# Optimization experiments

Measured on AMD Instinct MI355X. Metric: run time of the kernel, lower is better.

Reference implementation:

```python
import jax, jax.numpy as jnp
import numpy as np

B, L, D, H, E, K = 1, 512, 512, 512, 32, 2

def setup_inputs() -> dict:
    key = jax.random.key(0)
    ks = jax.random.split(key, 6)
    x = jax.random.normal(ks[0], (B, L, D), dtype=jnp.float32)
    router_scale = 1.0 + 0.02 * jax.random.normal(ks[1], (D,), dtype=jnp.float32)
    router_logits_w = 0.02 * jax.random.normal(ks[2], (D, E), dtype=jnp.float32)
    gating_einsum = 0.02 * jax.random.normal(ks[3], (E, 2, H, D), dtype=jnp.float32)
    linear_w = 0.02 * jax.random.normal(ks[4], (E, H, D), dtype=jnp.float32)
    per_expert_scale = 1.0 + 0.02 * jax.random.normal(ks[5], (E,), dtype=jnp.float32)
    return {"x": x, "router_scale": router_scale, "router_logits_w": router_logits_w,
            "gating_einsum": gating_einsum, "linear_w": linear_w,
            "per_expert_scale": per_expert_scale}

def reference(x, router_scale, router_logits_w, gating_einsum, linear_w, per_expert_scale):
    d = x.shape[-1]
    n_experts = router_logits_w.shape[-1]
    # RMSNorm without scale (fp32)
    x32 = x.astype(jnp.float32)
    var = jnp.mean(jnp.square(x32), axis=-1, keepdims=True)
    router_input = x32 * jax.lax.rsqrt(var + 1e-6)
    root_size = jax.lax.rsqrt(jnp.asarray(d, dtype=router_input.dtype))
    router_input = router_input * root_size * router_scale.astype(router_input.dtype)
    logits = jnp.dot(router_input, router_logits_w).astype(jnp.float32)  # [B,L,E]
    probs = jax.nn.softmax(logits, axis=-1)
    _, top_k_indices = jax.lax.top_k(logits, K)  # [B,L,K]
    indicator = jax.nn.one_hot(top_k_indices, n_experts, dtype=probs.dtype).sum(axis=-2)
    gate_weights = indicator * probs
    renorm = jnp.sum(gate_weights, axis=-1, keepdims=True)
    renorm = jnp.where(renorm > 0.0, renorm, 1.0)
    weights = probs / renorm
    top_k_weights = jnp.take_along_axis(weights, top_k_indices, axis=-1)  # [B,L,K]
    output = jnp.zeros_like(x)
    for ki in range(K):  # small fixed k; faithful to source's per-slot gather
        expert_idx = top_k_indices[:, :, ki]          # [B,L] int32
        expert_w = top_k_weights[:, :, ki]            # [B,L]
        gate_params = gating_einsum[expert_idx]       # [B,L,2,H,D] -- the big gather
        lin_params = linear_w[expert_idx]             # [B,L,H,D]
        escale = per_expert_scale[expert_idx]         # [B,L]
        gate_0 = jnp.einsum('bld,blhd->blh', x, gate_params[:, :, 0])
        gate_1 = jnp.einsum('bld,blhd->blh', x, gate_params[:, :, 1])
        activated = jax.nn.gelu(gate_0) * gate_1
        expert_out = jnp.einsum('blh,blhd->bld', activated, lin_params)
        output = output + expert_out * (escale * expert_w)[..., None]
    return output
```

## Files before the change

kernel.cpp:

```cpp
#include <hip/hip_runtime.h>
#include <hip/hip_bf16.h>
#include <math.h>

#define LTOK 512
#define DDIM 512
#define NEXP 32
#define HDIM 512

typedef __attribute__((ext_vector_type(8))) short short8;
typedef __attribute__((ext_vector_type(4))) float floatx4;

__device__ __forceinline__ unsigned bpack(float a, float b) {
    unsigned ua = __float_as_uint(a), ub = __float_as_uint(b);
    ua += 0x7FFFu + ((ua >> 16) & 1u);
    ub += 0x7FFFu + ((ub >> 16) & 1u);
    return (ua >> 16) | (ub & 0xFFFF0000u);
}


__global__ __launch_bounds__(64) void router_kernel(
    const float* __restrict__ x, const float* __restrict__ rs,
    const float* __restrict__ Wr, const float* __restrict__ pes,
    int* __restrict__ cnt, int* __restrict__ alist, float* __restrict__ slist,
    short* __restrict__ xb)
{
    const int t = blockIdx.x;
    const int lane = threadIdx.x;

    float xv[8];
    float ss = 0.f;
#pragma unroll
    for (int j = 0; j < 8; ++j) {
        xv[j] = x[t * DDIM + j * 64 + lane];
        ss += xv[j] * xv[j];
    }
#pragma unroll
    for (int j = 0; j < 8; ++j)
        xb[t * DDIM + j * 64 + lane] = (short)(bpack(xv[j], 0.f) & 0xFFFFu);

#pragma unroll
    for (int o = 32; o > 0; o >>= 1) ss += __shfl_xor(ss, o);
    const float var = ss * (1.0f / 512.0f);
    const float coef = rsqrtf(var + 1e-6f) * rsqrtf(512.0f);

    __shared__ float ri[DDIM];
#pragma unroll
    for (int j = 0; j < 8; ++j) {
        const int d = j * 64 + lane;
        ri[d] = xv[j] * coef * rs[d];
    }
    __syncthreads();

    const int e = lane & 31;
    const int half = lane >> 5;
    const int dbeg = half * 256;
    float l0 = 0.f, l1 = 0.f, l2 = 0.f, l3 = 0.f;
#pragma unroll 4
    for (int d = dbeg; d < dbeg + 256; d += 4) {
        l0 = fmaf(ri[d + 0], Wr[(d + 0) * NEXP + e], l0);
        l1 = fmaf(ri[d + 1], Wr[(d + 1) * NEXP + e], l1);
        l2 = fmaf(ri[d + 2], Wr[(d + 2) * NEXP + e], l2);
        l3 = fmaf(ri[d + 3], Wr[(d + 3) * NEXP + e], l3);
    }
    float lg = (l0 + l1) + (l2 + l3);
    lg += __shfl_xor(lg, 32);

    __shared__ float lgs[NEXP];
    if (lane < 32) lgs[lane] = lg;
    __syncthreads();

    if (lane == 0) {
        int i0 = 0; float m0 = lgs[0];
        for (int i = 1; i < NEXP; ++i) if (lgs[i] > m0) { m0 = lgs[i]; i0 = i; }
        int i1 = -1; float m1 = -1e30f;
        for (int i = 0; i < NEXP; ++i) if (i != i0 && lgs[i] > m1) { m1 = lgs[i]; i1 = i; }
        const float e1 = expf(m1 - m0);
        const float inv = 1.0f / (1.0f + e1);
        const float w0 = inv, w1 = e1 * inv;

        int p0 = atomicAdd(&cnt[i0], 1);
        alist[i0 * LTOK + p0] = t * 2;
        slist[i0 * LTOK + p0] = w0 * pes[i0];
        int p1 = atomicAdd(&cnt[i1], 1);
        alist[i1 * LTOK + p1] = t * 2 + 1;
        slist[i1 * LTOK + p1] = w1 * pes[i1];
    }
}

__global__ __launch_bounds__(256, 4) void gates_kernel(
    const short* __restrict__ xb, const float* __restrict__ G,
    const int* __restrict__ cnt, const int* __restrict__ alist,
    short* __restrict__ act)
{
    const int e  = blockIdx.y;
    const int h0 = blockIdx.x * 16;
    const int Ne = cnt[e];
    if (Ne == 0) return;
    const int wv   = threadIdx.x >> 6;
    const int g    = wv & 1;
    const int kh   = wv >> 1;
    const int lane = threadIdx.x & 63;
    const int n    = lane & 15;
    const int quad = lane >> 4;

    __shared__ float red[4][2][4][64];

    const float* Grow = G + ((size_t)((e * 2 + g) * HDIM) + h0 + n) * DDIM + kh * 256;
    const short* xbh  = xb + kh * 256;
    const int* al = alist + e * LTOK;

    short8 Bf[8];
#pragma unroll
    for (int ks = 0; ks < 8; ++ks) {
        const int ko = ks * 32 + quad * 8;
        const floatx4 b0 = *(const floatx4*)(Grow + ko);
        const floatx4 b1 = *(const floatx4*)(Grow + ko + 4);
        union { short8 s; unsigned u[4]; } B;
        B.u[0] = bpack(b0.x, b0.y);
        B.u[1] = bpack(b0.z, b0.w);
        B.u[2] = bpack(b1.x, b1.y);
        B.u[3] = bpack(b1.z, b1.w);
        Bf[ks] = B.s;
    }

    for (int mb = 0; mb < Ne; mb += 32) {
        int arow[2];
#pragma unroll
        for (int i = 0; i < 2; ++i) {
            int s = mb + i * 16 + n;
            arow[i] = al[s < Ne ? s : Ne - 1] >> 1;
        }
        floatx4 acc[2] = {};

#pragma unroll
        for (int ks = 0; ks < 8; ++ks) {
            const int ko = ks * 32 + quad * 8;
#pragma unroll
            for (int i = 0; i < 2; ++i) {
                const short8 A = *(const short8*)(xbh + (size_t)arow[i] * DDIM + ko);
                acc[i] = __builtin_amdgcn_mfma_f32_16x16x32_bf16(A, Bf[ks], acc[i], 0, 0, 0);
            }
        }

#pragma unroll
        for (int i = 0; i < 2; ++i)
#pragma unroll
            for (int r = 0; r < 4; ++r)
                red[wv][i][r][lane] = acc[i][r];
        __syncthreads();

        {
            const int i = wv & 1;
            const int u = wv >> 1;
#pragma unroll
            for (int rr = 0; rr < 2; ++rr) {
                const int r = u * 2 + rr;
                const int s = mb + i * 16 + quad * 4 + r;
                if (s < Ne) {
                    const int a = al[s];
                    const float g0 = red[0][i][r][lane] + red[2][i][r][lane];
                    const float g1 = red[1][i][r][lane] + red[3][i][r][lane];
                    const float uu = 0.7978845608f * (g0 + 0.044715f * g0 * g0 * g0);
                    const float sg = 1.0f / (1.0f + __expf(-2.0f * uu));
                    const float v = g0 * sg * g1;
                    act[(size_t)a * HDIM + h0 + n] = (short)(bpack(v, 0.f) & 0xFFFFu);
                }
            }
        }
        __syncthreads();
    }
}

__global__ __launch_bounds__(256, 4) void linear_kernel(
    const short* __restrict__ act, const float* __restrict__ Wl,
    const int* __restrict__ cnt, const int* __restrict__ alist,
    const float* __restrict__ slist, float* __restrict__ yb)
{
    const int e  = blockIdx.y;
    const int d0 = blockIdx.x * 16;
    const int Ne = cnt[e];
    if (Ne == 0) return;
    const int wv   = threadIdx.x >> 6;
    const int lane = threadIdx.x & 63;
    const int n    = lane & 15;
    const int quad = lane >> 4;

    __shared__ float red[4][2][4][64];

    const float* Wcol = Wl + (size_t)e * HDIM * DDIM + d0 + n;
    const int* al = alist + e * LTOK;
    const float* sl = slist + e * LTOK;

    short8 Bf[4];
#pragma unroll
    for (int ks = 0; ks < 4; ++ks) {
        const int ko = wv * 128 + ks * 32 + quad * 8;
        float w[8];
#pragma unroll
        for (int j = 0; j < 8; ++j)
            w[j] = Wcol[(size_t)(ko + j) * DDIM];
        union { short8 s; unsigned u[4]; } B;
        B.u[0] = bpack(w[0], w[1]);
        B.u[1] = bpack(w[2], w[3]);
        B.u[2] = bpack(w[4], w[5]);
        B.u[3] = bpack(w[6], w[7]);
        Bf[ks] = B.s;
    }

    for (int mb = 0; mb < Ne; mb += 32) {
        int arow[2];
#pragma unroll
        for (int i = 0; i < 2; ++i) {
            int s = mb + i * 16 + n;
            arow[i] = al[s < Ne ? s : Ne - 1];
        }
        floatx4 acc[2] = {};

#pragma unroll
        for (int ks = 0; ks < 4; ++ks) {
            const int ko = wv * 128 + ks * 32 + quad * 8;
#pragma unroll
            for (int i = 0; i < 2; ++i) {
                const short8 A = *(const short8*)(act + (size_t)arow[i] * HDIM + ko);
                acc[i] = __builtin_amdgcn_mfma_f32_16x16x32_bf16(A, Bf[ks], acc[i], 0, 0, 0);
            }
        }

#pragma unroll
        for (int i = 0; i < 2; ++i)
#pragma unroll
            for (int r = 0; r < 4; ++r)
                red[wv][i][r][lane] = acc[i][r];
        __syncthreads();

        {
            const int i = wv & 1;
            const int u = wv >> 1;
#pragma unroll
            for (int rr = 0; rr < 2; ++rr) {
                const int r = u * 2 + rr;
                const int s = mb + i * 16 + quad * 4 + r;
                if (s < Ne) {
                    const int a = al[s];
                    const float v = ((red[0][i][r][lane] + red[1][i][r][lane]) +
                                     (red[2][i][r][lane] + red[3][i][r][lane])) * sl[s];
                    yb[(size_t)a * DDIM + d0 + n] = v;
                }
            }
        }
        __syncthreads();
    }
}

__global__ __launch_bounds__(256) void combine_kernel(
    const float* __restrict__ yb, float* __restrict__ out)
{
    const int idx = blockIdx.x * 256 + threadIdx.x;
    const int t = idx >> 7, c = idx & 127;
    const floatx4 a = ((const floatx4*)(yb + (size_t)(2 * t) * DDIM))[c];
    const floatx4 b = ((const floatx4*)(yb + (size_t)(2 * t + 1) * DDIM))[c];
    ((floatx4*)(out + (size_t)t * DDIM))[c] = a + b;
}

extern "C" void kernel_launch(void* const* d_in, const int* in_sizes, int n_in,
                              void* d_out, int out_size, void* d_ws, size_t ws_size,
                              hipStream_t stream)
{
    const float* x   = (const float*)d_in[0];
    const float* rs  = (const float*)d_in[1];
    const float* Wr  = (const float*)d_in[2];
    const float* G   = (const float*)d_in[3];
    const float* Wl  = (const float*)d_in[4];
    const float* pes = (const float*)d_in[5];
    float* out = (float*)d_out;

    char* ws = (char*)d_ws;
    int*   cnt   = (int*)(ws);
    int*   alist = (int*)(ws + 256);
    float* slist = (float*)(ws + 256 + 65536);
    short* xb    = (short*)(ws + 131328);
    short* act   = (short*)(ws + 655616);
    float* yb    = (float*)(ws + 1704192);

    hipMemsetAsync(cnt, 0, NEXP * sizeof(int), stream);

    router_kernel<<<dim3(LTOK), dim3(64), 0, stream>>>(x, rs, Wr, pes, cnt, alist, slist, xb);
    gates_kernel<<<dim3(32, NEXP), dim3(256), 0, stream>>>(xb, G, cnt, alist, act);
    linear_kernel<<<dim3(32, NEXP), dim3(256), 0, stream>>>(act, Wl, cnt, alist, slist, yb);
    combine_kernel<<<dim3(256), dim3(256), 0, stream>>>(yb, out);
}
```

Baseline: 167.1 us.

## Drop memset and combine kernel; build per-expert token lists in LDS, atomically accumulate output

The router now writes each token's expert assignment and weight into flat arrays and zeroes the output. Gates and linear kernels each rebuild their expert's token list in shared memory by scanning the 1024 assignments. The linear kernel accumulates into the output with float atomics, so the memset and combine launches go away. The cost is a redundant scan in every block and atomic adds to global memory, which can make floating-point summation order nondeterministic.

```diff
diff --git a/kernel.cpp b/kernel.cpp
--- a/kernel.cpp
+++ b/kernel.cpp
@@ -21,8 +21,8 @@
 __global__ __launch_bounds__(64) void router_kernel(
     const float* __restrict__ x, const float* __restrict__ rs,
     const float* __restrict__ Wr, const float* __restrict__ pes,
-    int* __restrict__ cnt, int* __restrict__ alist, float* __restrict__ slist,
-    short* __restrict__ xb)
+    int* __restrict__ easgn, float* __restrict__ wts,
+    short* __restrict__ xb, float* __restrict__ out)
 {
     const int t = blockIdx.x;
     const int lane = threadIdx.x;
@@ -35,8 +35,10 @@
         ss += xv[j] * xv[j];
     }
 #pragma unroll
-    for (int j = 0; j < 8; ++j)
+    for (int j = 0; j < 8; ++j) {
         xb[t * DDIM + j * 64 + lane] = (short)(bpack(xv[j], 0.f) & 0xFFFFu);
+        out[t * DDIM + j * 64 + lane] = 0.f;
+    }
 
 #pragma unroll
     for (int o = 32; o > 0; o >>= 1) ss += __shfl_xor(ss, o);
@@ -76,38 +78,33 @@
         for (int i = 0; i < NEXP; ++i) if (i != i0 && lgs[i] > m1) { m1 = lgs[i]; i1 = i; }
         const float e1 = expf(m1 - m0);
         const float inv = 1.0f / (1.0f + e1);
-        const float w0 = inv, w1 = e1 * inv;
-
-        int p0 = atomicAdd(&cnt[i0], 1);
-        alist[i0 * LTOK + p0] = t * 2;
-        slist[i0 * LTOK + p0] = w0 * pes[i0];
-        int p1 = atomicAdd(&cnt[i1], 1);
-        alist[i1 * LTOK + p1] = t * 2 + 1;
-        slist[i1 * LTOK + p1] = w1 * pes[i1];
+        easgn[2 * t]     = i0;
+        easgn[2 * t + 1] = i1;
+        wts[2 * t]     = inv * pes[i0];
+        wts[2 * t + 1] = e1 * inv * pes[i1];
     }
 }
 
 __global__ __launch_bounds__(256, 4) void gates_kernel(
     const short* __restrict__ xb, const float* __restrict__ G,
-    const int* __restrict__ cnt, const int* __restrict__ alist,
-    short* __restrict__ act)
+    const int* __restrict__ easgn, short* __restrict__ act)
 {
     const int e  = blockIdx.y;
     const int h0 = blockIdx.x * 16;
-    const int Ne = cnt[e];
-    if (Ne == 0) return;
-    const int wv   = threadIdx.x >> 6;
+    const int tid = threadIdx.x;
+    const int wv   = tid >> 6;
     const int g    = wv & 1;
     const int kh   = wv >> 1;
-    const int lane = threadIdx.x & 63;
+    const int lane = tid & 63;
     const int n    = lane & 15;
     const int quad = lane >> 4;
 
+    __shared__ int toks[2 * LTOK];
+    __shared__ int lcnt;
     __shared__ float red[4][2][4][64];
 
     const float* Grow = G + ((size_t)((e * 2 + g) * HDIM) + h0 + n) * DDIM + kh * 256;
     const short* xbh  = xb + kh * 256;
-    const int* al = alist + e * LTOK;
 
     short8 Bf[8];
 #pragma unroll
@@ -123,12 +120,25 @@
         Bf[ks] = B.s;
     }
 
+    if (tid == 0) lcnt = 0;
+    __syncthreads();
+    {
+        const int4 eg = ((const int4*)easgn)[tid];
+        if (eg.x == e) { int p = atomicAdd(&lcnt, 1); toks[p] = 4 * tid; }
+        if (eg.y == e) { int p = atomicAdd(&lcnt, 1); toks[p] = 4 * tid + 1; }
+        if (eg.z == e) { int p = atomicAdd(&lcnt, 1); toks[p] = 4 * tid + 2; }
+        if (eg.w == e) { int p = atomicAdd(&lcnt, 1); toks[p] = 4 * tid + 3; }
+    }
+    __syncthreads();
+    const int Ne = lcnt;
+    if (Ne == 0) return;
+
     for (int mb = 0; mb < Ne; mb += 32) {
         int arow[2];
 #pragma unroll
         for (int i = 0; i < 2; ++i) {
             int s = mb + i * 16 + n;
-            arow[i] = al[s < Ne ? s : Ne - 1] >> 1;
+            arow[i] = toks[s < Ne ? s : Ne - 1] >> 1;
         }
         floatx4 acc[2] = {};
 
@@ -157,7 +167,7 @@
                 const int r = u * 2 + rr;
                 const int s = mb + i * 16 + quad * 4 + r;
                 if (s < Ne) {
-                    const int a = al[s];
+                    const int a = toks[s];
                     const float g0 = red[0][i][r][lane] + red[2][i][r][lane];
                     const float g1 = red[1][i][r][lane] + red[3][i][r][lane];
                     const float uu = 0.7978845608f * (g0 + 0.044715f * g0 * g0 * g0);
@@ -173,23 +183,22 @@
 
 __global__ __launch_bounds__(256, 4) void linear_kernel(
     const short* __restrict__ act, const float* __restrict__ Wl,
-    const int* __restrict__ cnt, const int* __restrict__ alist,
-    const float* __restrict__ slist, float* __restrict__ yb)
+    const int* __restrict__ easgn, const float* __restrict__ wts,
+    float* __restrict__ out)
 {
     const int e  = blockIdx.y;
     const int d0 = blockIdx.x * 16;
-    const int Ne = cnt[e];
-    if (Ne == 0) return;
-    const int wv   = threadIdx.x >> 6;
-    const int lane = threadIdx.x & 63;
+    const int tid = threadIdx.x;
+    const int wv   = tid >> 6;
+    const int lane = tid & 63;
     const int n    = lane & 15;
     const int quad = lane >> 4;
 
+    __shared__ int toks[2 * LTOK];
+    __shared__ int lcnt;
     __shared__ float red[4][2][4][64];
 
     const float* Wcol = Wl + (size_t)e * HDIM * DDIM + d0 + n;
-    const int* al = alist + e * LTOK;
-    const float* sl = slist + e * LTOK;
 
     short8 Bf[4];
 #pragma unroll
@@ -207,12 +216,25 @@
         Bf[ks] = B.s;
     }
 
+    if (tid == 0) lcnt = 0;
+    __syncthreads();
+    {
+        const int4 eg = ((const int4*)easgn)[tid];
+        if (eg.x == e) { int p = atomicAdd(&lcnt, 1); toks[p] = 4 * tid; }
+        if (eg.y == e) { int p = atomicAdd(&lcnt, 1); toks[p] = 4 * tid + 1; }
+        if (eg.z == e) { int p = atomicAdd(&lcnt, 1); toks[p] = 4 * tid + 2; }
+        if (eg.w == e) { int p = atomicAdd(&lcnt, 1); toks[p] = 4 * tid + 3; }
+    }
+    __syncthreads();
+    const int Ne = lcnt;
+    if (Ne == 0) return;
+
     for (int mb = 0; mb < Ne; mb += 32) {
         int arow[2];
 #pragma unroll
         for (int i = 0; i < 2; ++i) {
             int s = mb + i * 16 + n;
-            arow[i] = al[s < Ne ? s : Ne - 1];
+            arow[i] = toks[s < Ne ? s : Ne - 1];
         }
         floatx4 acc[2] = {};
 
@@ -241,25 +263,15 @@
                 const int r = u * 2 + rr;
                 const int s = mb + i * 16 + quad * 4 + r;
                 if (s < Ne) {
-                    const int a = al[s];
+                    const int slot = toks[s];
                     const float v = ((red[0][i][r][lane] + red[1][i][r][lane]) +
-                                     (red[2][i][r][lane] + red[3][i][r][lane])) * sl[s];
-                    yb[(size_t)a * DDIM + d0 + n] = v;
+                                     (red[2][i][r][lane] + red[3][i][r][lane])) * wts[slot];
+                    atomicAdd(&out[(size_t)(slot >> 1) * DDIM + d0 + n], v);
                 }
             }
         }
         __syncthreads();
     }
-}
-
-__global__ __launch_bounds__(256) void combine_kernel(
-    const float* __restrict__ yb, float* __restrict__ out)
-{
-    const int idx = blockIdx.x * 256 + threadIdx.x;
-    const int t = idx >> 7, c = idx & 127;
-    const floatx4 a = ((const floatx4*)(yb + (size_t)(2 * t) * DDIM))[c];
-    const floatx4 b = ((const floatx4*)(yb + (size_t)(2 * t + 1) * DDIM))[c];
-    ((floatx4*)(out + (size_t)t * DDIM))[c] = a + b;
 }
 
 extern "C" void kernel_launch(void* const* d_in, const int* in_sizes, int n_in,
@@ -275,17 +287,12 @@
     float* out = (float*)d_out;
 
     char* ws = (char*)d_ws;
-    int*   cnt   = (int*)(ws);
-    int*   alist = (int*)(ws + 256);
-    float* slist = (float*)(ws + 256 + 65536);
-    short* xb    = (short*)(ws + 131328);
-    short* act   = (short*)(ws + 655616);
-    float* yb    = (float*)(ws + 1704192);
-
-    hipMemsetAsync(cnt, 0, NEXP * sizeof(int), stream);
-
-    router_kernel<<<dim3(LTOK), dim3(64), 0, stream>>>(x, rs, Wr, pes, cnt, alist, slist, xb);
-    gates_kernel<<<dim3(32, NEXP), dim3(256), 0, stream>>>(xb, G, cnt, alist, act);
-    linear_kernel<<<dim3(32, NEXP), dim3(256), 0, stream>>>(act, Wl, cnt, alist, slist, yb);
-    combine_kernel<<<dim3(256), dim3(256), 0, stream>>>(yb, out);
-}
+    int*   easgn = (int*)(ws);
+    float* wts   = (float*)(ws + 4096);
+    short* xb    = (short*)(ws + 8192);
+    short* act   = (short*)(ws + 532480);
+
+    router_kernel<<<dim3(LTOK), dim3(64), 0, stream>>>(x, rs, Wr, pes, easgn, wts, xb, out);
+    gates_kernel<<<dim3(32, NEXP), dim3(256), 0, stream>>>(xb, G, easgn, act);
+    linear_kernel<<<dim3(32, NEXP), dim3(256), 0, stream>>>(act, Wl, easgn, wts, out);
+}
```

Result: faster. 158.3 us (-5.3%).
